# Kernel tuning notes

Hardware: AMD Instinct MI355X
Metric: run time of the kernel (lower is better)

The kernel has to match this reference:

```python
import jax, jax.numpy as jnp
import numpy as np

FP8_MAX = 448.0  # max finite value of float8_e4m3fn


def quantize_tensorwise(x):
    """Tensorwise fp8 quantization: returns fp8 tensor and inverse scale."""
    amax = jnp.max(jnp.abs(x))
    inv_scale = jnp.maximum(amax, jnp.asarray(1e-12, x.dtype)) / FP8_MAX
    q = (x / inv_scale).astype(jnp.float8_e4m3fn)
    return q, inv_scale


def setup_inputs() -> dict:
    key = jax.random.key(0)
    k1, k2, k3 = jax.random.split(key, 3)
    x = jax.random.normal(k1, (4, 1024, 4096), dtype=jnp.float32)
    weight = jax.random.normal(k2, (4096, 4096), dtype=jnp.float32) * 0.02
    bias = jax.random.normal(k3, (4096,), dtype=jnp.float32)
    return {"x": x, "weight": weight, "bias": bias}


def reference(x, weight, bias):
    out_shape = (*x.shape[:-1], weight.shape[0])
    xm = x.reshape(-1, x.shape[-1])                    # [M, K]
    fp8_x, x_inv_scale = quantize_tensorwise(xm)       # fp8 input + tensorwise scale
    fp8_wt, w_inv_scale = quantize_tensorwise(weight.T)  # weight.t() quantized, [K, N]
    # fp8 GEMM with inline dequant: (fp8_x @ fp8_w.T) * sx * sw + bias
    acc = jnp.matmul(fp8_x.astype(jnp.float32), fp8_wt.astype(jnp.float32))
    out = acc * (x_inv_scale * w_inv_scale) + bias.astype(jnp.float32)
    return out.reshape(out_shape).astype(x.dtype)
```

## Files before the change

### kernel.cpp

```cpp
#include <hip/hip_runtime.h>
#include <hip/hip_bf16.h>
#include <stdint.h>

static constexpr int M = 4096, N = 4096, K = 4096;
static constexpr float FP8_MAX = 448.0f;

using f32x4  = __attribute__((ext_vector_type(4))) float;
using f32x16 = __attribute__((ext_vector_type(16))) float;
using i32x4  = __attribute__((ext_vector_type(4))) int;
using i32x8  = __attribute__((ext_vector_type(8))) int;

static constexpr size_t AQ_OFF   = 0;
static constexpr size_t BQ_OFF   = (size_t)M * K;
static constexpr size_t AMAX_OFF = BQ_OFF + (size_t)N * K;

__global__ void init_amax_kernel(float* amax) {
    amax[0] = 0.0f;
    amax[1] = 0.0f;
}

__global__ __launch_bounds__(256) void amax_kernel(const float* __restrict__ x,
                                                   const float* __restrict__ w,
                                                   float* __restrict__ amax,
                                                   int n4_per_tensor,
                                                   int blocks_per_tensor) {
    const int tensor = blockIdx.x / blocks_per_tensor;
    const int blk    = blockIdx.x % blocks_per_tensor;
    const float4* src = (const float4*)(tensor == 0 ? x : w);

    float m = 0.0f;
    for (int i = blk * blockDim.x + threadIdx.x; i < n4_per_tensor;
         i += blocks_per_tensor * blockDim.x) {
        float4 v = src[i];
        m = fmaxf(m, fmaxf(fmaxf(fabsf(v.x), fabsf(v.y)),
                           fmaxf(fabsf(v.z), fabsf(v.w))));
    }
    #pragma unroll
    for (int off = 32; off >= 1; off >>= 1)
        m = fmaxf(m, __shfl_xor(m, off, 64));

    __shared__ float sm[4];
    const int lane = threadIdx.x & 63, wid = threadIdx.x >> 6;
    if (lane == 0) sm[wid] = m;
    __syncthreads();
    if (threadIdx.x == 0) {
        m = fmaxf(fmaxf(sm[0], sm[1]), fmaxf(sm[2], sm[3]));
        atomicMax((unsigned int*)&amax[tensor], __float_as_uint(m));
    }
}

__global__ __launch_bounds__(256) void quant_kernel(const float* __restrict__ x,
                                                    const float* __restrict__ w,
                                                    unsigned char* __restrict__ aq,
                                                    unsigned char* __restrict__ bq,
                                                    const float* __restrict__ amax,
                                                    int n4_per_tensor) {
    int gid = blockIdx.x * blockDim.x + threadIdx.x;
    const int tensor = (gid >= n4_per_tensor) ? 1 : 0;
    const int i = tensor ? gid - n4_per_tensor : gid;

    const float inv = fmaxf(amax[tensor], 1e-12f) / FP8_MAX;
    const float4* src = (const float4*)(tensor == 0 ? x : w);
    int* dst = (int*)(tensor == 0 ? aq : bq);

    float4 v = src[i];
    float q0 = v.x / inv, q1 = v.y / inv, q2 = v.z / inv, q3 = v.w / inv;
    int packed = __builtin_amdgcn_cvt_pk_fp8_f32(q0, q1, 0, false);
    packed     = __builtin_amdgcn_cvt_pk_fp8_f32(q2, q3, packed, true);
    dst[i] = packed;
}

static constexpr int BM = 128, BN = 128, BK = 64;

__device__ __forceinline__ void gld_lds16(const void* g, void* l) {
    __builtin_amdgcn_global_load_lds(
        (const __attribute__((address_space(1))) void*)g,
        (__attribute__((address_space(3))) void*)l, 16, 0, 0);
}

__global__ __launch_bounds__(256) void gemm_kernel(const unsigned char* __restrict__ Aq,
                                                   const unsigned char* __restrict__ Bq,
                                                   const float* __restrict__ amax,
                                                   const float* __restrict__ bias,
                                                   float* __restrict__ out) {
    __shared__ unsigned char Alds[BM * BK];
    __shared__ unsigned char Blds[BN * BK];

    const int tid  = threadIdx.x;
    const int lane = tid & 63;
    const int wid  = tid >> 6;
    const int brow = blockIdx.y * BM;
    const int bcol = blockIdx.x * BN;
    const int wr = wid >> 1, wc = wid & 1;

    const float sx = fmaxf(amax[0], 1e-12f) / FP8_MAX;
    const float sw = fmaxf(amax[1], 1e-12f) / FP8_MAX;
    const float scale = sx * sw;

    f32x16 acc[2][2] = {};

    const int seg0 = wid * 2, seg1 = wid * 2 + 1;
    const int srow  = lane >> 2;
    const int swz_s = (srow >> 1) & 3;
    const int scol  = ((lane & 3) ^ swz_s) * 16;
    const unsigned char* Abase = Aq + (size_t)brow * K;
    const unsigned char* Bbase = Bq + (size_t)bcol * K;

    const int frow = lane & 31;
    const int c0   = (lane >> 5) * 2;
    const int swzr = (frow >> 1) & 3;
    const int off0 = ((c0 ^ swzr) << 4);
    const int off1 = (((c0 + 1) ^ swzr) << 4);

    for (int k0 = 0; k0 < K; k0 += BK) {
        gld_lds16(Abase + (size_t)(seg0 * 16 + srow) * K + k0 + scol, &Alds[seg0 * 1024]);
        gld_lds16(Abase + (size_t)(seg1 * 16 + srow) * K + k0 + scol, &Alds[seg1 * 1024]);
        gld_lds16(Bbase + (size_t)(seg0 * 16 + srow) * K + k0 + scol, &Blds[seg0 * 1024]);
        gld_lds16(Bbase + (size_t)(seg1 * 16 + srow) * K + k0 + scol, &Blds[seg1 * 1024]);
        __syncthreads();

        i32x8 aF[2], bF[2];
        #pragma unroll
        for (int m = 0; m < 2; ++m) {
            const unsigned char* p = &Alds[(wr * 64 + m * 32 + frow) * BK];
            i32x4 lo = *(const i32x4*)(p + off0);
            i32x4 hi = *(const i32x4*)(p + off1);
            aF[m] = __builtin_shufflevector(lo, hi, 0, 1, 2, 3, 4, 5, 6, 7);
        }
        #pragma unroll
        for (int n = 0; n < 2; ++n) {
            const unsigned char* p = &Blds[(wc * 64 + n * 32 + frow) * BK];
            i32x4 lo = *(const i32x4*)(p + off0);
            i32x4 hi = *(const i32x4*)(p + off1);
            bF[n] = __builtin_shufflevector(lo, hi, 0, 1, 2, 3, 4, 5, 6, 7);
        }
        #pragma unroll
        for (int m = 0; m < 2; ++m)
            #pragma unroll
            for (int n = 0; n < 2; ++n)
                acc[m][n] = __builtin_amdgcn_mfma_scale_f32_32x32x64_f8f6f4(
                    aF[m], bF[n], acc[m][n],
                    0 , 0 ,
                    0, 0x7F , 0, 0x7F );
        __syncthreads();
    }

    #pragma unroll
    for (int m = 0; m < 2; ++m) {
        const int rbase = brow + wr * 64 + m * 32 + 4 * (lane >> 5);
        #pragma unroll
        for (int n = 0; n < 2; ++n) {
            const int col = bcol + wc * 64 + n * 32 + (lane & 31);
            const float b = bias[col];
            #pragma unroll
            for (int reg = 0; reg < 16; ++reg) {
                const int row = rbase + (reg & 3) + 8 * (reg >> 2);
                out[(size_t)row * N + col] = acc[m][n][reg] * scale + b;
            }
        }
    }
}

extern "C" void kernel_launch(void* const* d_in, const int* in_sizes, int n_in,
                              void* d_out, int out_size, void* d_ws, size_t ws_size,
                              hipStream_t stream) {
    const float* x    = (const float*)d_in[0];
    const float* w    = (const float*)d_in[1];
    const float* bias = (const float*)d_in[2];
    float* out = (float*)d_out;

    unsigned char* aq = (unsigned char*)d_ws + AQ_OFF;
    unsigned char* bq = (unsigned char*)d_ws + BQ_OFF;
    float* amax = (float*)((unsigned char*)d_ws + AMAX_OFF);

    const int n4 = (M * K) / 4;

    init_amax_kernel<<<1, 1, 0, stream>>>(amax);

    const int blocks_per_tensor = 512;
    amax_kernel<<<2 * blocks_per_tensor, 256, 0, stream>>>(x, w, amax, n4, blocks_per_tensor);

    const int quant_blocks = (2 * n4) / 256;
    quant_kernel<<<quant_blocks, 256, 0, stream>>>(x, w, aq, bq, amax, n4);

    dim3 grid(N / BN, M / BM);
    gemm_kernel<<<grid, 256, 0, stream>>>(aq, bq, amax, bias, out);
}
```

Measured before the change: 157.7 us.

## Enlarge GEMM tiles to 256x256 with 4-stage LDS pipeline and block swizzle

Reworks the fp8 GEMM to use 256x256 block tiles with 512 threads (8 waves, each computing 128x64) and a 4-deep LDS ring buffer filled by global_load_lds with explicit vmcnt waits. One barrier per K step replaces the previous load-sync-compute-sync loop. A block-index swizzle is added for L2 locality, and s_setprio is raised around the MFMA chain. The aim is to hide global load latency and increase data reuse per tile. The cost is 128KB of LDS and only 256 blocks, which may hurt occupancy and load balance across CUs.

```diff
diff --git a/kernel.cpp b/kernel.cpp
--- a/kernel.cpp
+++ b/kernel.cpp
@@ -5,7 +5,6 @@
 static constexpr int M = 4096, N = 4096, K = 4096;
 static constexpr float FP8_MAX = 448.0f;
 
-using f32x4  = __attribute__((ext_vector_type(4))) float;
 using f32x16 = __attribute__((ext_vector_type(16))) float;
 using i32x4  = __attribute__((ext_vector_type(4))) int;
 using i32x8  = __attribute__((ext_vector_type(8))) int;
@@ -70,7 +69,7 @@
     dst[i] = packed;
 }
 
-static constexpr int BM = 128, BN = 128, BK = 64;
+static constexpr int BM = 256, BN = 256, BK = 64, DEPTH = 4, NT = K / BK;
 
 __device__ __forceinline__ void gld_lds16(const void* g, void* l) {
     __builtin_amdgcn_global_load_lds(
@@ -78,84 +77,107 @@
         (__attribute__((address_space(3))) void*)l, 16, 0, 0);
 }
 
-__global__ __launch_bounds__(256) void gemm_kernel(const unsigned char* __restrict__ Aq,
-                                                   const unsigned char* __restrict__ Bq,
-                                                   const float* __restrict__ amax,
-                                                   const float* __restrict__ bias,
-                                                   float* __restrict__ out) {
-    __shared__ unsigned char Alds[BM * BK];
-    __shared__ unsigned char Blds[BN * BK];
+__global__ __launch_bounds__(512, 2) void gemm_kernel(const unsigned char* __restrict__ Aq,
+                                                      const unsigned char* __restrict__ Bq,
+                                                      const float* __restrict__ amax,
+                                                      const float* __restrict__ bias,
+                                                      float* __restrict__ out) {
+    __shared__ unsigned char lds[DEPTH][2][BM * BK];
 
     const int tid  = threadIdx.x;
     const int lane = tid & 63;
-    const int wid  = tid >> 6;
-    const int brow = blockIdx.y * BM;
-    const int bcol = blockIdx.x * BN;
-    const int wr = wid >> 1, wc = wid & 1;
+    const int w    = tid >> 6;
+    const int wr   = w >> 2, wc = w & 3;
+
+    const int bid = blockIdx.x;
+    const int swz = (bid & 7) * 32 + (bid >> 3);
+    const int brow = (swz >> 4) * BM;
+    const int bcol = (swz & 15) * BN;
 
     const float sx = fmaxf(amax[0], 1e-12f) / FP8_MAX;
     const float sw = fmaxf(amax[1], 1e-12f) / FP8_MAX;
     const float scale = sx * sw;
 
-    f32x16 acc[2][2] = {};
-
-    const int seg0 = wid * 2, seg1 = wid * 2 + 1;
-    const int srow  = lane >> 2;
-    const int swz_s = (srow >> 1) & 3;
-    const int scol  = ((lane & 3) ^ swz_s) * 16;
+    const int r4    = lane >> 2;
+    const int row0  = w * 16 + r4;
+    const int chk   = ((lane & 3) ^ ((row0 >> 1) & 3)) * 16;
     const unsigned char* Abase = Aq + (size_t)brow * K;
     const unsigned char* Bbase = Bq + (size_t)bcol * K;
 
     const int frow = lane & 31;
+    const int swzr = (frow >> 1) & 3;
     const int c0   = (lane >> 5) * 2;
-    const int swzr = (frow >> 1) & 3;
     const int off0 = ((c0 ^ swzr) << 4);
     const int off1 = (((c0 + 1) ^ swzr) << 4);
 
-    for (int k0 = 0; k0 < K; k0 += BK) {
-        gld_lds16(Abase + (size_t)(seg0 * 16 + srow) * K + k0 + scol, &Alds[seg0 * 1024]);
-        gld_lds16(Abase + (size_t)(seg1 * 16 + srow) * K + k0 + scol, &Alds[seg1 * 1024]);
-        gld_lds16(Bbase + (size_t)(seg0 * 16 + srow) * K + k0 + scol, &Blds[seg0 * 1024]);
-        gld_lds16(Bbase + (size_t)(seg1 * 16 + srow) * K + k0 + scol, &Blds[seg1 * 1024]);
-        __syncthreads();
-
-        i32x8 aF[2], bF[2];
-        #pragma unroll
-        for (int m = 0; m < 2; ++m) {
-            const unsigned char* p = &Alds[(wr * 64 + m * 32 + frow) * BK];
+    f32x16 acc[4][2] = {};
+
+#define STAGE(t, d)                                                              \
+    do {                                                                         \
+        const int _k0 = (t) * BK;                                                \
+        gld_lds16(Abase + (size_t)row0 * K + _k0 + chk,         &lds[d][0][w * 1024]);        \
+        gld_lds16(Abase + (size_t)(row0 + 128) * K + _k0 + chk, &lds[d][0][8192 + w * 1024]); \
+        gld_lds16(Bbase + (size_t)row0 * K + _k0 + chk,         &lds[d][1][w * 1024]);        \
+        gld_lds16(Bbase + (size_t)(row0 + 128) * K + _k0 + chk, &lds[d][1][8192 + w * 1024]); \
+    } while (0)
+
+    STAGE(0, 0);
+    STAGE(1, 1);
+    STAGE(2, 2);
+
+    for (int t = 0; t < NT; ++t) {
+        asm volatile("s_waitcnt vmcnt(8)" ::: "memory");
+        __builtin_amdgcn_s_barrier();
+
+        const int tn = (t + 3 < NT) ? t + 3 : NT - 1;
+        STAGE(tn, (t + 3) & 3);
+
+        const int d = t & 3;
+        const unsigned char* Ab = &lds[d][0][0];
+        const unsigned char* Bb = &lds[d][1][0];
+
+        i32x8 aF[4], bF[2];
+        #pragma unroll
+        for (int mt = 0; mt < 4; ++mt) {
+            const unsigned char* p = Ab + (wr * 128 + mt * 32 + frow) * BK;
             i32x4 lo = *(const i32x4*)(p + off0);
             i32x4 hi = *(const i32x4*)(p + off1);
-            aF[m] = __builtin_shufflevector(lo, hi, 0, 1, 2, 3, 4, 5, 6, 7);
+            aF[mt] = __builtin_shufflevector(lo, hi, 0, 1, 2, 3, 4, 5, 6, 7);
         }
         #pragma unroll
-        for (int n = 0; n < 2; ++n) {
-            const unsigned char* p = &Blds[(wc * 64 + n * 32 + frow) * BK];
+        for (int nt2 = 0; nt2 < 2; ++nt2) {
+            const unsigned char* p = Bb + (wc * 64 + nt2 * 32 + frow) * BK;
             i32x4 lo = *(const i32x4*)(p + off0);
             i32x4 hi = *(const i32x4*)(p + off1);
-            bF[n] = __builtin_shufflevector(lo, hi, 0, 1, 2, 3, 4, 5, 6, 7);
+            bF[nt2] = __builtin_shufflevector(lo, hi, 0, 1, 2, 3, 4, 5, 6, 7);
         }
-        #pragma unroll
-        for (int m = 0; m < 2; ++m)
+
+        __builtin_amdgcn_s_setprio(1);
+        #pragma unroll
+        for (int mt = 0; mt < 4; ++mt)
             #pragma unroll
-            for (int n = 0; n < 2; ++n)
-                acc[m][n] = __builtin_amdgcn_mfma_scale_f32_32x32x64_f8f6f4(
-                    aF[m], bF[n], acc[m][n],
-                    0 , 0 ,
-                    0, 0x7F , 0, 0x7F );
-        __syncthreads();
-    }
+            for (int nt2 = 0; nt2 < 2; ++nt2)
+                acc[mt][nt2] = __builtin_amdgcn_mfma_scale_f32_32x32x64_f8f6f4(
+                    aF[mt], bF[nt2], acc[mt][nt2],
+                    0, 0, 0, 0x7F, 0, 0x7F);
+        __builtin_amdgcn_s_setprio(0);
+
+        asm volatile("s_waitcnt lgkmcnt(0)" ::: "memory");
+        __builtin_amdgcn_sched_barrier(0);
+    }
+#undef STAGE
 
     #pragma unroll
-    for (int m = 0; m < 2; ++m) {
-        const int rbase = brow + wr * 64 + m * 32 + 4 * (lane >> 5);
-        #pragma unroll
-        for (int n = 0; n < 2; ++n) {
-            const int col = bcol + wc * 64 + n * 32 + (lane & 31);
+    for (int mt = 0; mt < 4; ++mt) {
+        const int rbase = brow + wr * 128 + mt * 32 + 4 * (lane >> 5);
+        #pragma unroll
+        for (int nt2 = 0; nt2 < 2; ++nt2) {
+            const int col = bcol + wc * 64 + nt2 * 32 + (lane & 31);
             const float b = bias[col];
             #pragma unroll
             for (int reg = 0; reg < 16; ++reg) {
                 const int row = rbase + (reg & 3) + 8 * (reg >> 2);
-                out[(size_t)row * N + col] = acc[m][n][reg] * scale + b;
+                out[(size_t)row * N + col] = acc[mt][nt2][reg] * scale + b;
             }
         }
     }
@@ -183,6 +205,5 @@
     const int quant_blocks = (2 * n4) / 256;
     quant_kernel<<<quant_blocks, 256, 0, stream>>>(x, w, aq, bq, amax, n4);
 
-    dim3 grid(N / BN, M / BM);
-    gemm_kernel<<<grid, 256, 0, stream>>>(aq, bq, amax, bias, out);
-}
+    gemm_kernel<<<256, 512, 0, stream>>>(aq, bq, amax, bias, out);
+}
```

Result: faster. 135.8 us (-13.9%).
